# Kernel tuning notes

Hardware: AMD Instinct MI355X
Metric: run time of the kernel (lower is better)

## Reference

```python
import jax, jax.numpy as jnp
import numpy as np
from jax import lax

B, T, D = 512, 1024, 64          # batch, timesteps, input_size
H, L, C = 32, 1, 4               # hidden_layer_size, latent_dim, categorical_dim
IN0 = D + L * C                  # lstm layer-0 input dim


def setup_inputs() -> dict:
    key = jax.random.key(0)
    ks = jax.random.split(key, 12)
    bound = 1.0 / np.sqrt(H)     # torch LSTM/Linear default uniform init
    u = lambda k, sh: jax.random.uniform(k, sh, jnp.float32, -bound, bound)

    states = jax.random.normal(ks[0], (B, T, D), jnp.float32)
    tau = jnp.float32(1.0)
    # pre-sampled standard Gumbel noise, time-major [T, B, L, C]
    un = jax.random.uniform(ks[1], (T, B, L, C), jnp.float32, 1e-6, 1.0 - 1e-6)
    gumbel = -jnp.log(-jnp.log(un))

    return {
        "states": states, "tau": tau, "gumbel": gumbel,
        # LSTM layer 0 (input = D + L*C)
        "w_ih0": u(ks[2], (4 * H, IN0)), "w_hh0": u(ks[3], (4 * H, H)),
        "b_ih0": u(ks[4], (4 * H,)),     "b_hh0": u(ks[5], (4 * H,)),
        # LSTM layer 1
        "w_ih1": u(ks[6], (4 * H, H)),   "w_hh1": u(ks[7], (4 * H, H)),
        "b_ih1": u(ks[8], (4 * H,)),     "b_hh1": u(ks[9], (4 * H,)),
        # output linear; bias initialized to eye(C)[0] per init_params
        "w_lin": u(ks[10], (L * C, H)),
        "b_lin": jnp.eye(C, dtype=jnp.float32)[0],
    }


def _lstm_cell(x, h, c, w_ih, w_hh, b_ih, b_hh):
    z = x @ w_ih.T + h @ w_hh.T + (b_ih + b_hh)   # [B, 4H], torch gate order i,f,g,o
    i, f, g, o = jnp.split(z, 4, axis=-1)
    c2 = jax.nn.sigmoid(f) * c + jax.nn.sigmoid(i) * jnp.tanh(g)
    h2 = jax.nn.sigmoid(o) * jnp.tanh(c2)
    return h2, c2


def reference(states, tau, gumbel, w_ih0, w_hh0, b_ih0, b_hh0,
              w_ih1, w_hh1, b_ih1, b_hh1, w_lin, b_lin):
    Bsz = states.shape[0]
    # init_states: zero hidden/cell, c_t = one-hot(0) tiled -> [B, L*C]
    c0 = jnp.tile(jnp.eye(C, dtype=states.dtype)[0], (Bsz, L))
    zeros = jnp.zeros((Bsz, H), states.dtype)
    carry0 = (zeros, zeros, zeros, zeros, c0)

    def step(carry, inp):
        h1, c1, h2, c2, ct = carry
        x_t, g_t = inp                                  # [B,D], [B,L,C]
        x = jnp.concatenate([x_t, ct], axis=-1)         # [B, D+L*C]
        h1, c1 = _lstm_cell(x, h1, c1, w_ih0, w_hh0, b_ih0, b_hh0)
        h2, c2 = _lstm_cell(h1, h2, c2, w_ih1, w_hh1, b_ih1, b_hh1)
        q = h2 @ w_lin.T + b_lin                        # [B, L*C]
        logits = q.reshape(Bsz, L, C)
        # soft gumbel-softmax (module in training mode -> hard=False)
        y = jax.nn.softmax((logits + g_t) / tau, axis=-1)
        ct = y.reshape(Bsz, L * C)
        return (h1, c1, h2, c2, ct), ct

    xs = (jnp.transpose(states, (1, 0, 2)), gumbel)     # time-major
    _, ys = lax.scan(step, carry0, xs)                  # [T, B, L*C]
    return jnp.transpose(ys, (1, 0, 2))                 # [B, T, L*C]
```

## Files before the change

kernel.cpp:

```cpp
#include <hip/hip_runtime.h>

#define BB 512
#define TT 1024
#define DD 64
#define HH 32
#define CC 4
#define TILE 16
#define NT (TT / TILE)

typedef float f4 __attribute__((ext_vector_type(4)));
typedef _Float16 hv2 __attribute__((ext_vector_type(2)));

__device__ __forceinline__ float rcpf(float x) { return __builtin_amdgcn_rcpf(x); }
__device__ __forceinline__ float sigm(float x) { return rcpf(1.0f + __expf(-x)); }
__device__ __forceinline__ float tanh_f(float x) {
    return 1.0f - 2.0f * rcpf(__expf(2.0f * x) + 1.0f);
}
__device__ __forceinline__ float pk2(float a, float b) {
    hv2 t; t.x = (_Float16)a; t.y = (_Float16)b;
    return __builtin_bit_cast(float, t);
}
__device__ __forceinline__ hv2 bch(float x) { return __builtin_bit_cast(hv2, x); }
__device__ __forceinline__ float fdot2(float w, float h, float c) {
    return __builtin_amdgcn_fdot2(bch(w), bch(h), c, false);
}

#define DOT32(a0, a1, a2, a3, W, H4)                    \
    _Pragma("unroll")                                   \
    for (int k2 = 0; k2 < 4; ++k2) {                    \
        f4 h_ = H4[k2];                                 \
        a0 = fdot2(W[4 * k2 + 0], h_.x, a0);            \
        a1 = fdot2(W[4 * k2 + 1], h_.y, a1);            \
        a2 = fdot2(W[4 * k2 + 2], h_.z, a2);            \
        a3 = fdot2(W[4 * k2 + 3], h_.w, a3);            \
    }

#define COMBINE(zA, zB, zi, zf, zg, zo)                 \
    {                                                   \
        float pA_ = __shfl_xor(zA, 32, 64);             \
        float pB_ = __shfl_xor(zB, 32, 64);             \
        zi = half ? pA_ : zA; zf = half ? zA : pA_;     \
        zg = half ? pB_ : zB; zo = half ? zB : pB_;     \
    }

__global__ void __launch_bounds__(128, 4)
zx_gemm(const float* __restrict__ states,
        const float* __restrict__ w_ih0,
        const float* __restrict__ b_ih0,
        const float* __restrict__ b_hh0,
        float* __restrict__ zx)
{
    const int b = blockIdx.y;
    const int tile = blockIdx.x;
    const int tid = threadIdx.x;
    __shared__ __align__(16) float xs[16][DD];

    const int tbase = tile * 16;
#pragma unroll
    for (int i = 0; i < 2; ++i) {
        int f = i * 128 + tid;
        int row = f >> 4, c4 = f & 15;
        int t = tbase + row; if (t > TT - 1) t = TT - 1;
        ((f4*)xs)[f] = *(const f4*)(states + ((size_t)b * TT + t) * DD + c4 * 4);
    }
    __syncthreads();

    const int r = tid;
    const f4* wr = (const f4*)(w_ih0 + (size_t)r * 68);
    f4 w[16];
#pragma unroll
    for (int k = 0; k < 16; ++k) w[k] = wr[k];
    const float bias = b_ih0[r] + b_hh0[r];

    for (int i = 0; i < 16; ++i) {
        int t = tbase + i;
        if (t >= TT) break;
        const f4* xv = (const f4*)xs[i];
        float a0 = bias, a1 = 0.f, a2 = 0.f, a3 = 0.f;
#pragma unroll
        for (int k = 0; k < 16; ++k) {
            f4 x4 = xv[k];
            a0 = fmaf(w[k].x, x4.x, a0);
            a1 = fmaf(w[k].y, x4.y, a1);
            a2 = fmaf(w[k].z, x4.z, a2);
            a3 = fmaf(w[k].w, x4.w, a3);
        }
        zx[((size_t)b * TT + t) * 128 + r] = (a0 + a1) + (a2 + a3);
    }
}

__global__ void __launch_bounds__(64, 1)
lstm_pipe(const float* __restrict__ zx,
          const float* __restrict__ taup,
          const float* __restrict__ gumbel,
          const float* __restrict__ w_ih0,
          const float* __restrict__ w_hh0,
          const float* __restrict__ w_ih1,
          const float* __restrict__ w_hh1,
          const float* __restrict__ b_ih1,
          const float* __restrict__ b_hh1,
          const float* __restrict__ w_lin,
          const float* __restrict__ b_lin,
          float* __restrict__ out)
{
    const int b    = blockIdx.x;
    const int l    = threadIdx.x;
    const int half = l >> 5;
    const int rA   = l;
    const int rB   = l + 64;
    const int c    = l >> 4;

    __shared__ __align__(16) float zbuf[2][TILE][128];
    __shared__ __align__(16) float4 gbuf[2][TILE];
    __shared__ __align__(16) _Float16 h1h[HH];
    __shared__ __align__(16) _Float16 h2h[HH];

    f4 wctA = *(const f4*)(w_ih0 + (size_t)rA * 68 + 64);
    f4 wctB = *(const f4*)(w_ih0 + (size_t)rB * 68 + 64);
    float wh0A[16], wh0B[16], wi1A[16], wi1B[16], wh1A[16], wh1B[16], wlc[16];
#pragma unroll
    for (int k = 0; k < 8; ++k) {
        f4 w;
        w = *(const f4*)(w_hh0 + (size_t)rA * HH + 4 * k);
        wh0A[2 * k] = pk2(w.x, w.y); wh0A[2 * k + 1] = pk2(w.z, w.w);
        w = *(const f4*)(w_hh0 + (size_t)rB * HH + 4 * k);
        wh0B[2 * k] = pk2(w.x, w.y); wh0B[2 * k + 1] = pk2(w.z, w.w);
        w = *(const f4*)(w_ih1 + (size_t)rA * HH + 4 * k);
        wi1A[2 * k] = pk2(w.x, w.y); wi1A[2 * k + 1] = pk2(w.z, w.w);
        w = *(const f4*)(w_ih1 + (size_t)rB * HH + 4 * k);
        wi1B[2 * k] = pk2(w.x, w.y); wi1B[2 * k + 1] = pk2(w.z, w.w);
        w = *(const f4*)(w_hh1 + (size_t)rA * HH + 4 * k);
        wh1A[2 * k] = pk2(w.x, w.y); wh1A[2 * k + 1] = pk2(w.z, w.w);
        w = *(const f4*)(w_hh1 + (size_t)rB * HH + 4 * k);
        wh1B[2 * k] = pk2(w.x, w.y); wh1B[2 * k + 1] = pk2(w.z, w.w);
        w = *(const f4*)(w_lin + (size_t)c * HH + 4 * k);
        wlc[2 * k] = pk2(w.x, w.y); wlc[2 * k + 1] = pk2(w.z, w.w);
    }
    const float bias1A = b_ih1[rA] + b_hh1[rA];
    const float bias1B = b_ih1[rB] + b_hh1[rB];
    const float inv_tau = rcpf(taup[0]);
    const float blc = b_lin[c];

    const float* __restrict__ zb = zx + (size_t)b * TT * 128;
    float* __restrict__ ob = out + (size_t)b * TT * CC;
    const int srow = l >> 5;
    const int scol = l & 31;

    {
        f4 sz[8];
#pragma unroll
        for (int i = 0; i < 8; ++i) {
            int row = 1 + i * 2 + srow;
            sz[i] = *(const f4*)(zb + (size_t)row * 128 + scol * 4);
        }
        float4 gv = *(const float4*)(gumbel + ((size_t)(l & 15) * BB + b) * CC);
#pragma unroll
        for (int i = 0; i < 8; ++i) ((f4*)&zbuf[0][0][0])[i * 64 + l] = sz[i];
        if (l < 16) gbuf[0][l] = gv;
    }

    float cst1 = 0.f, cst2 = 0.f;
    f4 h1g[4];

    {
        float zA = zb[rA] + wctA.x;
        float zB = zb[rB] + wctB.x;
        float zi, zf, zg, zo;
        COMBINE(zA, zB, zi, zf, zg, zo);
        (void)zf;
        cst1 = sigm(zi) * tanh_f(zg);
        float h1n = sigm(zo) * tanh_f(cst1);
        if (l < HH) h1h[l] = (_Float16)h1n;
#pragma unroll
        for (int k2 = 0; k2 < 4; ++k2) h1g[k2] = ((const f4*)h1h)[k2];

        float bA0 = bias1A, bA1 = 0.f, bA2 = 0.f, bA3 = 0.f;
        float bB0 = bias1B, bB1 = 0.f, bB2 = 0.f, bB3 = 0.f;
        DOT32(bA0, bA1, bA2, bA3, wi1A, h1g);
        DOT32(bB0, bB1, bB2, bB3, wi1B, h1g);
        zA = (bA0 + bA1) + (bA2 + bA3);
        zB = (bB0 + bB1) + (bB2 + bB3);
        COMBINE(zA, zB, zi, zf, zg, zo);
        cst2 = sigm(zi) * tanh_f(zg);
        float h2n = sigm(zo) * tanh_f(cst2);
        if (l < HH) h2h[l] = (_Float16)h2n;
    }

    for (int k = 0; k < NT; ++k) {
        const int cb = k & 1, nb = cb ^ 1;
        const int kn = (k + 1 < NT) ? k + 1 : 0;
        float4 gv;

#pragma unroll
        for (int hf = 0; hf < 2; ++hf) {
            f4 szh[4];
#pragma unroll
            for (int i = 0; i < 4; ++i) {
                int ii = hf * 4 + i;
                int row = kn * TILE + 1 + ii * 2 + srow;
                if (row > TT - 1) row = TT - 1;
                szh[i] = *(const f4*)(zb + (size_t)row * 128 + scol * 4);
            }
            if (hf == 0)
                gv = *(const float4*)(gumbel +
                        ((size_t)(kn * TILE + (l & 15)) * BB + b) * CC);

#pragma unroll 2
            for (int s8 = 0; s8 < 8; ++s8) {
                const int s = hf * 8 + s8;
                const int t = k * TILE + s;

                const float zxnA = zbuf[cb][s][rA];
                const float zxnB = zbuf[cb][s][rB];
                const float4 gtc = gbuf[cb][s];
                f4 h2g[4];
#pragma unroll
                for (int k2 = 0; k2 < 4; ++k2) h2g[k2] = ((const f4*)h2h)[k2];

                float aA0 = 0.f, aA1 = 0.f, aA2 = 0.f, aA3 = 0.f;
                float aB0 = 0.f, aB1 = 0.f, aB2 = 0.f, aB3 = 0.f;
                DOT32(aA0, aA1, aA2, aA3, wh0A, h1g);
                DOT32(aB0, aB1, aB2, aB3, wh0B, h1g);

                float s0 = blc, s1 = 0.f, s2 = 0.f, s3 = 0.f;
                DOT32(s0, s1, s2, s3, wlc, h2g);
                float qown = (s0 + s1) + (s2 + s3);

                float t1 = __shfl_xor(qown, 16, 64);
                float t2 = __shfl_xor(qown, 32, 64);
                float t3 = __shfl_xor(qown, 48, 64);
                float q0 = (c == 0) ? qown : (c == 1) ? t1 : (c == 2) ? t2 : t3;
                float q1 = (c == 0) ? t1 : (c == 1) ? qown : (c == 2) ? t3 : t2;
                float q2 = (c == 0) ? t2 : (c == 1) ? t3 : (c == 2) ? qown : t1;
                float q3 = (c == 0) ? t3 : (c == 1) ? t2 : (c == 2) ? t1 : qown;
                float l0  = (q0 + gtc.x) * inv_tau;
                float l1_ = (q1 + gtc.y) * inv_tau;
                float l2  = (q2 + gtc.z) * inv_tau;
                float l3  = (q3 + gtc.w) * inv_tau;
                float m = fmaxf(fmaxf(l0, l1_), fmaxf(l2, l3));
                float e0 = __expf(l0 - m), e1 = __expf(l1_ - m);
                float e2 = __expf(l2 - m), e3 = __expf(l3 - m);
                float inv = rcpf((e0 + e1) + (e2 + e3));
                float y0 = e0 * inv, y1 = e1 * inv, y2 = e2 * inv, y3 = e3 * inv;
                if (l == 0)
                    *(float4*)(ob + (size_t)t * CC) = make_float4(y0, y1, y2, y3);

                aA0 += zxnA; aB0 += zxnB;
                aA0 = fmaf(wctA.x, y0, aA0); aA1 = fmaf(wctA.y, y1, aA1);
                aA2 = fmaf(wctA.z, y2, aA2); aA3 = fmaf(wctA.w, y3, aA3);
                aB0 = fmaf(wctB.x, y0, aB0); aB1 = fmaf(wctB.y, y1, aB1);
                aB2 = fmaf(wctB.z, y2, aB2); aB3 = fmaf(wctB.w, y3, aB3);
                float zA = (aA0 + aA1) + (aA2 + aA3);
                float zB = (aB0 + aB1) + (aB2 + aB3);
                float zi, zf, zg, zo;
                COMBINE(zA, zB, zi, zf, zg, zo);
                cst1 = sigm(zf) * cst1 + sigm(zi) * tanh_f(zg);
                float h1n = sigm(zo) * tanh_f(cst1);
                if (l < HH) h1h[l] = (_Float16)h1n;

#pragma unroll
                for (int k2 = 0; k2 < 4; ++k2) h1g[k2] = ((const f4*)h1h)[k2];

                float bA0 = bias1A, bA1 = 0.f, bA2 = 0.f, bA3 = 0.f;
                float bB0 = bias1B, bB1 = 0.f, bB2 = 0.f, bB3 = 0.f;
                DOT32(bA0, bA1, bA2, bA3, wh1A, h2g);
                DOT32(bB0, bB1, bB2, bB3, wh1B, h2g);
                DOT32(bA0, bA1, bA2, bA3, wi1A, h1g);
                DOT32(bB0, bB1, bB2, bB3, wi1B, h1g);
                zA = (bA0 + bA1) + (bA2 + bA3);
                zB = (bB0 + bB1) + (bB2 + bB3);
                COMBINE(zA, zB, zi, zf, zg, zo);
                cst2 = sigm(zf) * cst2 + sigm(zi) * tanh_f(zg);
                float h2n = sigm(zo) * tanh_f(cst2);
                if (l < HH) h2h[l] = (_Float16)h2n;
            }

#pragma unroll
            for (int i = 0; i < 4; ++i)
                ((f4*)&zbuf[nb][0][0])[(hf * 4 + i) * 64 + l] = szh[i];
        }
        if (l < 16) gbuf[nb][l] = gv;

        asm volatile("" : "+v"(wh0A[0]), "+v"(wh0A[1]), "+v"(wh0A[2]), "+v"(wh0A[3]),
                          "+v"(wh0A[4]), "+v"(wh0A[5]), "+v"(wh0A[6]), "+v"(wh0A[7]),
                          "+v"(wh0A[8]), "+v"(wh0A[9]), "+v"(wh0A[10]), "+v"(wh0A[11]),
                          "+v"(wh0A[12]), "+v"(wh0A[13]), "+v"(wh0A[14]), "+v"(wh0A[15]));
        asm volatile("" : "+v"(wh0B[0]), "+v"(wh0B[1]), "+v"(wh0B[2]), "+v"(wh0B[3]),
                          "+v"(wh0B[4]), "+v"(wh0B[5]), "+v"(wh0B[6]), "+v"(wh0B[7]),
                          "+v"(wh0B[8]), "+v"(wh0B[9]), "+v"(wh0B[10]), "+v"(wh0B[11]),
                          "+v"(wh0B[12]), "+v"(wh0B[13]), "+v"(wh0B[14]), "+v"(wh0B[15]));
        asm volatile("" : "+v"(wi1A[0]), "+v"(wi1A[1]), "+v"(wi1A[2]), "+v"(wi1A[3]),
                          "+v"(wi1A[4]), "+v"(wi1A[5]), "+v"(wi1A[6]), "+v"(wi1A[7]),
                          "+v"(wi1A[8]), "+v"(wi1A[9]), "+v"(wi1A[10]), "+v"(wi1A[11]),
                          "+v"(wi1A[12]), "+v"(wi1A[13]), "+v"(wi1A[14]), "+v"(wi1A[15]));
        asm volatile("" : "+v"(wi1B[0]), "+v"(wi1B[1]), "+v"(wi1B[2]), "+v"(wi1B[3]),
                          "+v"(wi1B[4]), "+v"(wi1B[5]), "+v"(wi1B[6]), "+v"(wi1B[7]),
                          "+v"(wi1B[8]), "+v"(wi1B[9]), "+v"(wi1B[10]), "+v"(wi1B[11]),
                          "+v"(wi1B[12]), "+v"(wi1B[13]), "+v"(wi1B[14]), "+v"(wi1B[15]));
        asm volatile("" : "+v"(wh1A[0]), "+v"(wh1A[1]), "+v"(wh1A[2]), "+v"(wh1A[3]),
                          "+v"(wh1A[4]), "+v"(wh1A[5]), "+v"(wh1A[6]), "+v"(wh1A[7]),
                          "+v"(wh1A[8]), "+v"(wh1A[9]), "+v"(wh1A[10]), "+v"(wh1A[11]),
                          "+v"(wh1A[12]), "+v"(wh1A[13]), "+v"(wh1A[14]), "+v"(wh1A[15]));
        asm volatile("" : "+v"(wh1B[0]), "+v"(wh1B[1]), "+v"(wh1B[2]), "+v"(wh1B[3]),
                          "+v"(wh1B[4]), "+v"(wh1B[5]), "+v"(wh1B[6]), "+v"(wh1B[7]),
                          "+v"(wh1B[8]), "+v"(wh1B[9]), "+v"(wh1B[10]), "+v"(wh1B[11]),
                          "+v"(wh1B[12]), "+v"(wh1B[13]), "+v"(wh1B[14]), "+v"(wh1B[15]));
        asm volatile("" : "+v"(wlc[0]), "+v"(wlc[1]), "+v"(wlc[2]), "+v"(wlc[3]),
                          "+v"(wlc[4]), "+v"(wlc[5]), "+v"(wlc[6]), "+v"(wlc[7]),
                          "+v"(wlc[8]), "+v"(wlc[9]), "+v"(wlc[10]), "+v"(wlc[11]),
                          "+v"(wlc[12]), "+v"(wlc[13]), "+v"(wlc[14]), "+v"(wlc[15]));
        asm volatile("" : "+v"(wctA), "+v"(wctB));
    }
}

extern "C" __global__ void __launch_bounds__(128, 2)
lstm_opt_enc(const float* __restrict__ states, const float* __restrict__ taup,
             const float* __restrict__ gumbel, const float* __restrict__ w_ih0,
             const float* __restrict__ w_hh0, const float* __restrict__ b_ih0,
             const float* __restrict__ b_hh0, const float* __restrict__ w_ih1,
             const float* __restrict__ w_hh1, const float* __restrict__ b_ih1,
             const float* __restrict__ b_hh1, const float* __restrict__ w_lin,
             const float* __restrict__ b_lin, float* __restrict__ out)
{
    const int b   = blockIdx.x;
    const int tid = threadIdx.x;
    const int l   = tid & 63;
    const int wv  = tid >> 6;
    const int u0  = l & 15;
    const int g   = l >> 4;
    const int u   = wv * 16 + u0;
    const int r   = g * 32 + u;

    __shared__ __align__(16) float xb[2][DD];
    __shared__ __align__(16) float h1b[2][HH];
    __shared__ __align__(16) float h2b[2][HH];

    float wi0r[68], wh0r[HH], wi1r[HH], wh1r[HH];
#pragma unroll
    for (int k = 0; k < 68; ++k) wi0r[k] = w_ih0[r * 68 + k];
#pragma unroll
    for (int k = 0; k < HH; ++k) wh0r[k] = w_hh0[r * HH + k];
#pragma unroll
    for (int k = 0; k < HH; ++k) wi1r[k] = w_ih1[r * HH + k];
#pragma unroll
    for (int k = 0; k < HH; ++k) wh1r[k] = w_hh1[r * HH + k];
    const float bias0 = b_ih0[r] + b_hh0[r];
    const float bias1 = b_ih1[r] + b_hh1[r];
    const float inv_tau = rcpf(taup[0]);
    const float wl0 = w_lin[g * HH + u0];
    const float wl1 = w_lin[g * HH + u0 + 16];
    const float blc = b_lin[g];

    float cst1 = 0.f, cst2 = 0.f;
    float y0 = 1.f, y1 = 0.f, y2 = 0.f, y3 = 0.f;

    const float* __restrict__ sb = states + (size_t)b * TT * DD;
    float* __restrict__ ob = out + (size_t)b * TT * CC;

    float xr = 0.f;
    if (tid < DD) xr = sb[tid];
    if (tid < HH) { h1b[0][tid] = 0.f; h2b[0][tid] = 0.f; }
    if (tid < DD) { xb[0][tid] = xr; xr = sb[DD + tid]; }
    __syncthreads();

    for (int t = 0; t < TT; ++t) {
        const int p = t & 1, np = p ^ 1;
        if (tid < DD) { xb[np][tid] = xr; }
        const int tn = (t + 2 < TT) ? t + 2 : TT - 1;
        if (tid < DD) { xr = sb[tn * DD + tid]; }
        const float4 gt = *(const float4*)(gumbel + ((size_t)t * BB + b) * CC);

        float a0 = bias0, a1 = 0.f, a2 = 0.f, a3 = 0.f;
        const float4* xv = (const float4*)xb[p];
#pragma unroll
        for (int k = 0; k < 16; ++k) {
            float4 x4 = xv[k];
            a0 = fmaf(wi0r[4 * k + 0], x4.x, a0);
            a1 = fmaf(wi0r[4 * k + 1], x4.y, a1);
            a2 = fmaf(wi0r[4 * k + 2], x4.z, a2);
            a3 = fmaf(wi0r[4 * k + 3], x4.w, a3);
        }
        a0 = fmaf(wi0r[64], y0, a0);
        a1 = fmaf(wi0r[65], y1, a1);
        a2 = fmaf(wi0r[66], y2, a2);
        a3 = fmaf(wi0r[67], y3, a3);
        const float4* h1v = (const float4*)h1b[p];
#pragma unroll
        for (int k = 0; k < 8; ++k) {
            float4 h4 = h1v[k];
            a0 = fmaf(wh0r[4 * k + 0], h4.x, a0);
            a1 = fmaf(wh0r[4 * k + 1], h4.y, a1);
            a2 = fmaf(wh0r[4 * k + 2], h4.z, a2);
            a3 = fmaf(wh0r[4 * k + 3], h4.w, a3);
        }
        float z = (a0 + a1) + (a2 + a3);
        float v1  = __shfl_xor(z, 16, 64);
        float lo  = (g & 1) ? v1 : z;
        float hi  = (g & 1) ? z  : v1;
        float lo2 = __shfl_xor(lo, 32, 64);
        float hi2 = __shfl_xor(hi, 32, 64);
        float zi = (g < 2) ? lo  : lo2;
        float zf = (g < 2) ? hi  : hi2;
        float zg = (g < 2) ? lo2 : lo;
        float zo = (g < 2) ? hi2 : hi;
        cst1 = sigm(zf) * cst1 + sigm(zi) * tanh_f(zg);
        float h1new = sigm(zo) * tanh_f(cst1);
        if (g == 0) h1b[np][u] = h1new;
        __syncthreads();

        a0 = bias1; a1 = 0.f; a2 = 0.f; a3 = 0.f;
        const float4* h1n = (const float4*)h1b[np];
        const float4* h2v = (const float4*)h2b[p];
#pragma unroll
        for (int k = 0; k < 8; ++k) {
            float4 h4 = h1n[k];
            float4 g4 = h2v[k];
            a0 = fmaf(wi1r[4 * k + 0], h4.x, a0);
            a1 = fmaf(wi1r[4 * k + 1], h4.y, a1);
            a2 = fmaf(wi1r[4 * k + 2], h4.z, a2);
            a3 = fmaf(wi1r[4 * k + 3], h4.w, a3);
            a0 = fmaf(wh1r[4 * k + 0], g4.x, a0);
            a1 = fmaf(wh1r[4 * k + 1], g4.y, a1);
            a2 = fmaf(wh1r[4 * k + 2], g4.z, a2);
            a3 = fmaf(wh1r[4 * k + 3], g4.w, a3);
        }
        z = (a0 + a1) + (a2 + a3);
        v1  = __shfl_xor(z, 16, 64);
        lo  = (g & 1) ? v1 : z;
        hi  = (g & 1) ? z  : v1;
        lo2 = __shfl_xor(lo, 32, 64);
        hi2 = __shfl_xor(hi, 32, 64);
        zi = (g < 2) ? lo  : lo2;
        zf = (g < 2) ? hi  : hi2;
        zg = (g < 2) ? lo2 : lo;
        zo = (g < 2) ? hi2 : hi;
        cst2 = sigm(zf) * cst2 + sigm(zi) * tanh_f(zg);
        float h2new = sigm(zo) * tanh_f(cst2);
        if (g == 0) h2b[np][u] = h2new;
        __syncthreads();

        float part = wl0 * h2b[np][u0] + wl1 * h2b[np][u0 + 16];
        part += __shfl_xor(part, 1, 64);
        part += __shfl_xor(part, 2, 64);
        part += __shfl_xor(part, 4, 64);
        part += __shfl_xor(part, 8, 64);
        float qown = part + blc;
        float t1 = __shfl_xor(qown, 16, 64);
        float t2 = __shfl_xor(qown, 32, 64);
        float t3 = __shfl_xor(t1, 32, 64);
        float q0 = (g == 0) ? qown : (g == 1) ? t1 : (g == 2) ? t2 : t3;
        float q1 = (g == 0) ? t1 : (g == 1) ? qown : (g == 2) ? t3 : t2;
        float q2 = (g == 0) ? t2 : (g == 1) ? t3 : (g == 2) ? qown : t1;
        float q3 = (g == 0) ? t3 : (g == 1) ? t2 : (g == 2) ? t1 : qown;
        float l0  = (q0 + gt.x) * inv_tau;
        float l1_ = (q1 + gt.y) * inv_tau;
        float l2  = (q2 + gt.z) * inv_tau;
        float l3  = (q3 + gt.w) * inv_tau;
        float m = fmaxf(fmaxf(l0, l1_), fmaxf(l2, l3));
        float e0 = __expf(l0 - m), e1 = __expf(l1_ - m);
        float e2 = __expf(l2 - m), e3 = __expf(l3 - m);
        float inv = rcpf((e0 + e1) + (e2 + e3));
        y0 = e0 * inv; y1 = e1 * inv; y2 = e2 * inv; y3 = e3 * inv;

        if (tid == 0) *(float4*)(ob + (size_t)t * CC) = make_float4(y0, y1, y2, y3);
    }
}

extern "C" void kernel_launch(void* const* d_in, const int* in_sizes, int n_in,
                              void* d_out, int out_size, void* d_ws, size_t ws_size,
                              hipStream_t stream) {
    const float* states = (const float*)d_in[0];
    const float* tau    = (const float*)d_in[1];
    const float* gumbel = (const float*)d_in[2];
    const float* w_ih0  = (const float*)d_in[3];
    const float* w_hh0  = (const float*)d_in[4];
    const float* b_ih0  = (const float*)d_in[5];
    const float* b_hh0  = (const float*)d_in[6];
    const float* w_ih1  = (const float*)d_in[7];
    const float* w_hh1  = (const float*)d_in[8];
    const float* b_ih1  = (const float*)d_in[9];
    const float* b_hh1  = (const float*)d_in[10];
    const float* w_lin  = (const float*)d_in[11];
    const float* b_lin  = (const float*)d_in[12];
    float* out = (float*)d_out;

    const size_t zx_bytes = (size_t)BB * TT * 128 * 4;
    if (ws_size >= zx_bytes) {
        float* zx = (float*)d_ws;
        hipLaunchKernelGGL(zx_gemm, dim3(NT, BB), dim3(128), 0, stream,
                           states, w_ih0, b_ih0, b_hh0, zx);
        hipLaunchKernelGGL(lstm_pipe, dim3(BB), dim3(64), 0, stream,
                           zx, tau, gumbel, w_ih0, w_hh0, w_ih1, w_hh1,
                           b_ih1, b_hh1, w_lin, b_lin, out);
    } else {
        hipLaunchKernelGGL(lstm_opt_enc, dim3(BB), dim3(128), 0, stream,
                           states, tau, gumbel, w_ih0, w_hh0, b_ih0, b_hh0,
                           w_ih1, w_hh1, b_ih1, b_hh1, w_lin, b_lin, out);
    }
}
```

Measured before the change: 948.9 us.

## Fold log2(e) into weights and replace LDS tile staging with register prefetch

Pre-scales all gate weights, biases, the precomputed input projection and the output linear weights by log2(e) (and 1/tau), so sigmoid, tanh and softmax can call exp2 directly without a multiply on each call. Drops the double-buffered shared-memory staging of zx and gumbel tiles. Instead each lane prefetches its own zx gate values and the gumbel vector a few timesteps ahead into small register rings. The softmax normalisation is also folded into the layer-0 input FMA. This shortens the per-step serial dependency chain but gives up coalesced tile loads for scalar per-step global loads and slightly changes rounding.

```diff
diff --git a/kernel.cpp b/kernel.cpp
--- a/kernel.cpp
+++ b/kernel.cpp
@@ -5,16 +5,20 @@
 #define DD 64
 #define HH 32
 #define CC 4
-#define TILE 16
-#define NT (TT / TILE)
 
 typedef float f4 __attribute__((ext_vector_type(4)));
 typedef _Float16 hv2 __attribute__((ext_vector_type(2)));
 
+#define LOG2E 1.4426950408889634f
+#define TWO_LOG2E 2.8853900817779268f
+
 __device__ __forceinline__ float rcpf(float x) { return __builtin_amdgcn_rcpf(x); }
-__device__ __forceinline__ float sigm(float x) { return rcpf(1.0f + __expf(-x)); }
-__device__ __forceinline__ float tanh_f(float x) {
-    return 1.0f - 2.0f * rcpf(__expf(2.0f * x) + 1.0f);
+__device__ __forceinline__ float sigm2(float x) { return rcpf(1.0f + exp2f(-x)); }
+__device__ __forceinline__ float tanh2(float x) {
+    return 1.0f - 2.0f * rcpf(exp2f(x + x) + 1.0f);
+}
+__device__ __forceinline__ float tanh_c(float c) {
+    return 1.0f - 2.0f * rcpf(exp2f(c * TWO_LOG2E) + 1.0f);
 }
 __device__ __forceinline__ float pk2(float a, float b) {
     hv2 t; t.x = (_Float16)a; t.y = (_Float16)b;
@@ -85,7 +89,7 @@
             a2 = fmaf(w[k].z, x4.z, a2);
             a3 = fmaf(w[k].w, x4.w, a3);
         }
-        zx[((size_t)b * TT + t) * 128 + r] = (a0 + a1) + (a2 + a3);
+        zx[((size_t)b * TT + t) * 128 + r] = ((a0 + a1) + (a2 + a3)) * LOG2E;
     }
 }
 
@@ -110,54 +114,40 @@
     const int rB   = l + 64;
     const int c    = l >> 4;
 
-    __shared__ __align__(16) float zbuf[2][TILE][128];
-    __shared__ __align__(16) float4 gbuf[2][TILE];
     __shared__ __align__(16) _Float16 h1h[HH];
     __shared__ __align__(16) _Float16 h2h[HH];
 
+    const float inv_tau = rcpf(taup[0]);
+    const float gs = LOG2E * inv_tau;
+
     f4 wctA = *(const f4*)(w_ih0 + (size_t)rA * 68 + 64);
     f4 wctB = *(const f4*)(w_ih0 + (size_t)rB * 68 + 64);
+    wctA *= LOG2E; wctB *= LOG2E;
     float wh0A[16], wh0B[16], wi1A[16], wi1B[16], wh1A[16], wh1B[16], wlc[16];
 #pragma unroll
     for (int k = 0; k < 8; ++k) {
         f4 w;
-        w = *(const f4*)(w_hh0 + (size_t)rA * HH + 4 * k);
+        w = *(const f4*)(w_hh0 + (size_t)rA * HH + 4 * k) * LOG2E;
         wh0A[2 * k] = pk2(w.x, w.y); wh0A[2 * k + 1] = pk2(w.z, w.w);
-        w = *(const f4*)(w_hh0 + (size_t)rB * HH + 4 * k);
+        w = *(const f4*)(w_hh0 + (size_t)rB * HH + 4 * k) * LOG2E;
         wh0B[2 * k] = pk2(w.x, w.y); wh0B[2 * k + 1] = pk2(w.z, w.w);
-        w = *(const f4*)(w_ih1 + (size_t)rA * HH + 4 * k);
+        w = *(const f4*)(w_ih1 + (size_t)rA * HH + 4 * k) * LOG2E;
         wi1A[2 * k] = pk2(w.x, w.y); wi1A[2 * k + 1] = pk2(w.z, w.w);
-        w = *(const f4*)(w_ih1 + (size_t)rB * HH + 4 * k);
+        w = *(const f4*)(w_ih1 + (size_t)rB * HH + 4 * k) * LOG2E;
         wi1B[2 * k] = pk2(w.x, w.y); wi1B[2 * k + 1] = pk2(w.z, w.w);
-        w = *(const f4*)(w_hh1 + (size_t)rA * HH + 4 * k);
+        w = *(const f4*)(w_hh1 + (size_t)rA * HH + 4 * k) * LOG2E;
         wh1A[2 * k] = pk2(w.x, w.y); wh1A[2 * k + 1] = pk2(w.z, w.w);
-        w = *(const f4*)(w_hh1 + (size_t)rB * HH + 4 * k);
+        w = *(const f4*)(w_hh1 + (size_t)rB * HH + 4 * k) * LOG2E;
         wh1B[2 * k] = pk2(w.x, w.y); wh1B[2 * k + 1] = pk2(w.z, w.w);
-        w = *(const f4*)(w_lin + (size_t)c * HH + 4 * k);
+        w = *(const f4*)(w_lin + (size_t)c * HH + 4 * k) * gs;
         wlc[2 * k] = pk2(w.x, w.y); wlc[2 * k + 1] = pk2(w.z, w.w);
     }
-    const float bias1A = b_ih1[rA] + b_hh1[rA];
-    const float bias1B = b_ih1[rB] + b_hh1[rB];
-    const float inv_tau = rcpf(taup[0]);
-    const float blc = b_lin[c];
+    const float bias1A = (b_ih1[rA] + b_hh1[rA]) * LOG2E;
+    const float bias1B = (b_ih1[rB] + b_hh1[rB]) * LOG2E;
+    const float blc = b_lin[c] * gs;
 
     const float* __restrict__ zb = zx + (size_t)b * TT * 128;
     float* __restrict__ ob = out + (size_t)b * TT * CC;
-    const int srow = l >> 5;
-    const int scol = l & 31;
-
-    {
-        f4 sz[8];
-#pragma unroll
-        for (int i = 0; i < 8; ++i) {
-            int row = 1 + i * 2 + srow;
-            sz[i] = *(const f4*)(zb + (size_t)row * 128 + scol * 4);
-        }
-        float4 gv = *(const float4*)(gumbel + ((size_t)(l & 15) * BB + b) * CC);
-#pragma unroll
-        for (int i = 0; i < 8; ++i) ((f4*)&zbuf[0][0][0])[i * 64 + l] = sz[i];
-        if (l < 16) gbuf[0][l] = gv;
-    }
 
     float cst1 = 0.f, cst2 = 0.f;
     f4 h1g[4];
@@ -168,8 +158,8 @@
         float zi, zf, zg, zo;
         COMBINE(zA, zB, zi, zf, zg, zo);
         (void)zf;
-        cst1 = sigm(zi) * tanh_f(zg);
-        float h1n = sigm(zo) * tanh_f(cst1);
+        cst1 = sigm2(zi) * tanh2(zg);
+        float h1n = sigm2(zo) * tanh_c(cst1);
         if (l < HH) h1h[l] = (_Float16)h1n;
 #pragma unroll
         for (int k2 = 0; k2 < 4; ++k2) h1g[k2] = ((const f4*)h1h)[k2];
@@ -181,105 +171,103 @@
         zA = (bA0 + bA1) + (bA2 + bA3);
         zB = (bB0 + bB1) + (bB2 + bB3);
         COMBINE(zA, zB, zi, zf, zg, zo);
-        cst2 = sigm(zi) * tanh_f(zg);
-        float h2n = sigm(zo) * tanh_f(cst2);
+        cst2 = sigm2(zi) * tanh2(zg);
+        float h2n = sigm2(zo) * tanh_c(cst2);
         if (l < HH) h2h[l] = (_Float16)h2n;
     }
 
-    for (int k = 0; k < NT; ++k) {
-        const int cb = k & 1, nb = cb ^ 1;
-        const int kn = (k + 1 < NT) ? k + 1 : 0;
-        float4 gv;
-
-#pragma unroll
-        for (int hf = 0; hf < 2; ++hf) {
-            f4 szh[4];
-#pragma unroll
-            for (int i = 0; i < 4; ++i) {
-                int ii = hf * 4 + i;
-                int row = kn * TILE + 1 + ii * 2 + srow;
-                if (row > TT - 1) row = TT - 1;
-                szh[i] = *(const f4*)(zb + (size_t)row * 128 + scol * 4);
+    float zsA[4], zsB[4];
+    float4 gsl[2];
+#pragma unroll
+    for (int p = 0; p < 2; ++p) {
+        int row = p + 1; if (row > TT - 1) row = TT - 1;
+        zsA[p] = zb[(size_t)row * 128 + rA];
+        zsB[p] = zb[(size_t)row * 128 + rB];
+        gsl[p] = *(const float4*)(gumbel + ((size_t)p * BB + b) * CC);
+    }
+
+    for (int tk = 0; tk < TT / 8; ++tk) {
+#pragma unroll
+        for (int s = 0; s < 8; ++s) {
+            const int t = tk * 8 + s;
+            const int sl = s & 3;
+
+            const float zxnA = zsA[sl];
+            const float zxnB = zsB[sl];
+            const float4 graw = gsl[s & 1];
+
+            {
+                int rowz = t + 3; if (rowz > TT - 1) rowz = TT - 1;
+                zsA[(s + 2) & 3] = zb[(size_t)rowz * 128 + rA];
+                zsB[(s + 2) & 3] = zb[(size_t)rowz * 128 + rB];
+                int rowg = t + 2; if (rowg > TT - 1) rowg = TT - 1;
+                gsl[s & 1] = *(const float4*)(gumbel + ((size_t)rowg * BB + b) * CC);
             }
-            if (hf == 0)
-                gv = *(const float4*)(gumbel +
-                        ((size_t)(kn * TILE + (l & 15)) * BB + b) * CC);
-
-#pragma unroll 2
-            for (int s8 = 0; s8 < 8; ++s8) {
-                const int s = hf * 8 + s8;
-                const int t = k * TILE + s;
-
-                const float zxnA = zbuf[cb][s][rA];
-                const float zxnB = zbuf[cb][s][rB];
-                const float4 gtc = gbuf[cb][s];
-                f4 h2g[4];
-#pragma unroll
-                for (int k2 = 0; k2 < 4; ++k2) h2g[k2] = ((const f4*)h2h)[k2];
-
-                float aA0 = 0.f, aA1 = 0.f, aA2 = 0.f, aA3 = 0.f;
-                float aB0 = 0.f, aB1 = 0.f, aB2 = 0.f, aB3 = 0.f;
-                DOT32(aA0, aA1, aA2, aA3, wh0A, h1g);
-                DOT32(aB0, aB1, aB2, aB3, wh0B, h1g);
-
-                float s0 = blc, s1 = 0.f, s2 = 0.f, s3 = 0.f;
-                DOT32(s0, s1, s2, s3, wlc, h2g);
-                float qown = (s0 + s1) + (s2 + s3);
-
-                float t1 = __shfl_xor(qown, 16, 64);
-                float t2 = __shfl_xor(qown, 32, 64);
-                float t3 = __shfl_xor(qown, 48, 64);
-                float q0 = (c == 0) ? qown : (c == 1) ? t1 : (c == 2) ? t2 : t3;
-                float q1 = (c == 0) ? t1 : (c == 1) ? qown : (c == 2) ? t3 : t2;
-                float q2 = (c == 0) ? t2 : (c == 1) ? t3 : (c == 2) ? qown : t1;
-                float q3 = (c == 0) ? t3 : (c == 1) ? t2 : (c == 2) ? t1 : qown;
-                float l0  = (q0 + gtc.x) * inv_tau;
-                float l1_ = (q1 + gtc.y) * inv_tau;
-                float l2  = (q2 + gtc.z) * inv_tau;
-                float l3  = (q3 + gtc.w) * inv_tau;
-                float m = fmaxf(fmaxf(l0, l1_), fmaxf(l2, l3));
-                float e0 = __expf(l0 - m), e1 = __expf(l1_ - m);
-                float e2 = __expf(l2 - m), e3 = __expf(l3 - m);
-                float inv = rcpf((e0 + e1) + (e2 + e3));
-                float y0 = e0 * inv, y1 = e1 * inv, y2 = e2 * inv, y3 = e3 * inv;
-                if (l == 0)
-                    *(float4*)(ob + (size_t)t * CC) = make_float4(y0, y1, y2, y3);
-
-                aA0 += zxnA; aB0 += zxnB;
-                aA0 = fmaf(wctA.x, y0, aA0); aA1 = fmaf(wctA.y, y1, aA1);
-                aA2 = fmaf(wctA.z, y2, aA2); aA3 = fmaf(wctA.w, y3, aA3);
-                aB0 = fmaf(wctB.x, y0, aB0); aB1 = fmaf(wctB.y, y1, aB1);
-                aB2 = fmaf(wctB.z, y2, aB2); aB3 = fmaf(wctB.w, y3, aB3);
-                float zA = (aA0 + aA1) + (aA2 + aA3);
-                float zB = (aB0 + aB1) + (aB2 + aB3);
-                float zi, zf, zg, zo;
-                COMBINE(zA, zB, zi, zf, zg, zo);
-                cst1 = sigm(zf) * cst1 + sigm(zi) * tanh_f(zg);
-                float h1n = sigm(zo) * tanh_f(cst1);
-                if (l < HH) h1h[l] = (_Float16)h1n;
-
-#pragma unroll
-                for (int k2 = 0; k2 < 4; ++k2) h1g[k2] = ((const f4*)h1h)[k2];
-
-                float bA0 = bias1A, bA1 = 0.f, bA2 = 0.f, bA3 = 0.f;
-                float bB0 = bias1B, bB1 = 0.f, bB2 = 0.f, bB3 = 0.f;
-                DOT32(bA0, bA1, bA2, bA3, wh1A, h2g);
-                DOT32(bB0, bB1, bB2, bB3, wh1B, h2g);
-                DOT32(bA0, bA1, bA2, bA3, wi1A, h1g);
-                DOT32(bB0, bB1, bB2, bB3, wi1B, h1g);
-                zA = (bA0 + bA1) + (bA2 + bA3);
-                zB = (bB0 + bB1) + (bB2 + bB3);
-                COMBINE(zA, zB, zi, zf, zg, zo);
-                cst2 = sigm(zf) * cst2 + sigm(zi) * tanh_f(zg);
-                float h2n = sigm(zo) * tanh_f(cst2);
-                if (l < HH) h2h[l] = (_Float16)h2n;
-            }
-
-#pragma unroll
-            for (int i = 0; i < 4; ++i)
-                ((f4*)&zbuf[nb][0][0])[(hf * 4 + i) * 64 + l] = szh[i];
+
+            f4 h2g[4];
+#pragma unroll
+            for (int k2 = 0; k2 < 4; ++k2) h2g[k2] = ((const f4*)h2h)[k2];
+
+            float aA0 = 0.f, aA1 = 0.f, aA2 = 0.f, aA3 = 0.f;
+            float aB0 = 0.f, aB1 = 0.f, aB2 = 0.f, aB3 = 0.f;
+            DOT32(aA0, aA1, aA2, aA3, wh0A, h1g);
+            DOT32(aB0, aB1, aB2, aB3, wh0B, h1g);
+
+            float s0 = blc, s1 = 0.f, s2 = 0.f, s3 = 0.f;
+            DOT32(s0, s1, s2, s3, wlc, h2g);
+            float qown = (s0 + s1) + (s2 + s3);
+
+            float t1 = __shfl_xor(qown, 16, 64);
+            float t2 = __shfl_xor(qown, 32, 64);
+            float t3 = __shfl_xor(qown, 48, 64);
+            float q0 = (c == 0) ? qown : (c == 1) ? t1 : (c == 2) ? t2 : t3;
+            float q1 = (c == 0) ? t1 : (c == 1) ? qown : (c == 2) ? t3 : t2;
+            float q2 = (c == 0) ? t2 : (c == 1) ? t3 : (c == 2) ? qown : t1;
+            float q3 = (c == 0) ? t3 : (c == 1) ? t2 : (c == 2) ? t1 : qown;
+            float l0 = fmaf(graw.x, gs, q0);
+            float l1_ = fmaf(graw.y, gs, q1);
+            float l2 = fmaf(graw.z, gs, q2);
+            float l3 = fmaf(graw.w, gs, q3);
+            float m = fmaxf(fmaxf(l0, l1_), fmaxf(l2, l3));
+            float e0 = exp2f(l0 - m), e1 = exp2f(l1_ - m);
+            float e2 = exp2f(l2 - m), e3 = exp2f(l3 - m);
+            float inv = rcpf((e0 + e1) + (e2 + e3));
+            if (l == 0)
+                *(float4*)(ob + (size_t)t * CC) =
+                    make_float4(e0 * inv, e1 * inv, e2 * inv, e3 * inv);
+
+            float weA0 = wctA.x * e0, weA1 = wctA.y * e1;
+            float weA2 = wctA.z * e2, weA3 = wctA.w * e3;
+            float weB0 = wctB.x * e0, weB1 = wctB.y * e1;
+            float weB2 = wctB.z * e2, weB3 = wctB.w * e3;
+            aA0 = fmaf(weA0, inv, aA0 + zxnA); aA1 = fmaf(weA1, inv, aA1);
+            aA2 = fmaf(weA2, inv, aA2);        aA3 = fmaf(weA3, inv, aA3);
+            aB0 = fmaf(weB0, inv, aB0 + zxnB); aB1 = fmaf(weB1, inv, aB1);
+            aB2 = fmaf(weB2, inv, aB2);        aB3 = fmaf(weB3, inv, aB3);
+            float zA = (aA0 + aA1) + (aA2 + aA3);
+            float zB = (aB0 + aB1) + (aB2 + aB3);
+            float zi, zf, zg, zo;
+            COMBINE(zA, zB, zi, zf, zg, zo);
+            cst1 = fmaf(sigm2(zf), cst1, sigm2(zi) * tanh2(zg));
+            float h1n = sigm2(zo) * tanh_c(cst1);
+            if (l < HH) h1h[l] = (_Float16)h1n;
+
+#pragma unroll
+            for (int k2 = 0; k2 < 4; ++k2) h1g[k2] = ((const f4*)h1h)[k2];
+
+            float bA0 = bias1A, bA1 = 0.f, bA2 = 0.f, bA3 = 0.f;
+            float bB0 = bias1B, bB1 = 0.f, bB2 = 0.f, bB3 = 0.f;
+            DOT32(bA0, bA1, bA2, bA3, wh1A, h2g);
+            DOT32(bB0, bB1, bB2, bB3, wh1B, h2g);
+            DOT32(bA0, bA1, bA2, bA3, wi1A, h1g);
+            DOT32(bB0, bB1, bB2, bB3, wi1B, h1g);
+            zA = (bA0 + bA1) + (bA2 + bA3);
+            zB = (bB0 + bB1) + (bB2 + bB3);
+            COMBINE(zA, zB, zi, zf, zg, zo);
+            cst2 = fmaf(sigm2(zf), cst2, sigm2(zi) * tanh2(zg));
+            float h2n = sigm2(zo) * tanh_c(cst2);
+            if (l < HH) h2h[l] = (_Float16)h2n;
         }
-        if (l < 16) gbuf[nb][l] = gv;
 
         asm volatile("" : "+v"(wh0A[0]), "+v"(wh0A[1]), "+v"(wh0A[2]), "+v"(wh0A[3]),
                           "+v"(wh0A[4]), "+v"(wh0A[5]), "+v"(wh0A[6]), "+v"(wh0A[7]),
@@ -346,7 +334,7 @@
     for (int k = 0; k < HH; ++k) wh1r[k] = w_hh1[r * HH + k];
     const float bias0 = b_ih0[r] + b_hh0[r];
     const float bias1 = b_ih1[r] + b_hh1[r];
-    const float inv_tau = rcpf(taup[0]);
+    const float inv_tau = __builtin_amdgcn_rcpf(taup[0]);
     const float wl0 = w_lin[g * HH + u0];
     const float wl1 = w_lin[g * HH + u0 + 16];
     const float blc = b_lin[g];
@@ -403,8 +391,12 @@
         float zf = (g < 2) ? hi  : hi2;
         float zg = (g < 2) ? lo2 : lo;
         float zo = (g < 2) ? hi2 : hi;
-        cst1 = sigm(zf) * cst1 + sigm(zi) * tanh_f(zg);
-        float h1new = sigm(zo) * tanh_f(cst1);
+        float sf = __builtin_amdgcn_rcpf(1.0f + __expf(-zf));
+        float si = __builtin_amdgcn_rcpf(1.0f + __expf(-zi));
+        float tg = 1.0f - 2.0f * __builtin_amdgcn_rcpf(__expf(2.0f * zg) + 1.0f);
+        float so = __builtin_amdgcn_rcpf(1.0f + __expf(-zo));
+        cst1 = sf * cst1 + si * tg;
+        float h1new = so * (1.0f - 2.0f * __builtin_amdgcn_rcpf(__expf(2.0f * cst1) + 1.0f));
         if (g == 0) h1b[np][u] = h1new;
         __syncthreads();
 
@@ -434,8 +426,12 @@
         zf = (g < 2) ? hi  : hi2;
         zg = (g < 2) ? lo2 : lo;
         zo = (g < 2) ? hi2 : hi;
-        cst2 = sigm(zf) * cst2 + sigm(zi) * tanh_f(zg);
-        float h2new = sigm(zo) * tanh_f(cst2);
+        sf = __builtin_amdgcn_rcpf(1.0f + __expf(-zf));
+        si = __builtin_amdgcn_rcpf(1.0f + __expf(-zi));
+        tg = 1.0f - 2.0f * __builtin_amdgcn_rcpf(__expf(2.0f * zg) + 1.0f);
+        so = __builtin_amdgcn_rcpf(1.0f + __expf(-zo));
+        cst2 = sf * cst2 + si * tg;
+        float h2new = so * (1.0f - 2.0f * __builtin_amdgcn_rcpf(__expf(2.0f * cst2) + 1.0f));
         if (g == 0) h2b[np][u] = h2new;
         __syncthreads();
 
@@ -459,7 +455,7 @@
         float m = fmaxf(fmaxf(l0, l1_), fmaxf(l2, l3));
         float e0 = __expf(l0 - m), e1 = __expf(l1_ - m);
         float e2 = __expf(l2 - m), e3 = __expf(l3 - m);
-        float inv = rcpf((e0 + e1) + (e2 + e3));
+        float inv = __builtin_amdgcn_rcpf((e0 + e1) + (e2 + e3));
         y0 = e0 * inv; y1 = e1 * inv; y2 = e2 * inv; y3 = e3 * inv;
 
         if (tid == 0) *(float4*)(ob + (size_t)t * CC) = make_float4(y0, y1, y2, y3);
@@ -487,7 +483,7 @@
     const size_t zx_bytes = (size_t)BB * TT * 128 * 4;
     if (ws_size >= zx_bytes) {
         float* zx = (float*)d_ws;
-        hipLaunchKernelGGL(zx_gemm, dim3(NT, BB), dim3(128), 0, stream,
+        hipLaunchKernelGGL(zx_gemm, dim3(TT / 16, BB), dim3(128), 0, stream,
                            states, w_ih0, b_ih0, b_hh0, zx);
         hipLaunchKernelGGL(lstm_pipe, dim3(BB), dim3(64), 0, stream,
                            zx, tau, gumbel, w_ih0, w_hh0, w_ih1, w_hh1,
```

Result: slower. 1.264 ms (+33.3%).
